# Optimization experiments

Measured on AMD Instinct MI355X. Metric: run time of the kernel, lower is better.

The kernel has to match this reference:

```python
import jax, jax.numpy as jnp
import numpy as np
import math

N_NODES = 50000
N_EDGES = 640000
IN_FEATS = 128
HEADS = 8
OUT_FEATS = 16
D_FF = 4 * IN_FEATS


def setup_inputs() -> dict:
    key = jax.random.key(0)
    ks = jax.random.split(key, 10)
    s = 0.05
    return {
        "feat": jax.random.normal(ks[0], (N_NODES, IN_FEATS), jnp.float32),
        "src": jax.random.randint(ks[1], (N_EDGES,), 0, N_NODES, jnp.int32),
        "dst": jax.random.randint(ks[2], (N_EDGES,), 0, N_NODES, jnp.int32),
        "Wq": jax.random.normal(ks[3], (IN_FEATS, HEADS * OUT_FEATS), jnp.float32) * s,
        "Wk": jax.random.normal(ks[4], (IN_FEATS, HEADS * OUT_FEATS), jnp.float32) * s,
        "Wv": jax.random.normal(ks[5], (IN_FEATS, HEADS * OUT_FEATS), jnp.float32) * s,
        "ln1_g": jnp.ones((IN_FEATS,), jnp.float32),
        "ln1_b": jnp.zeros((IN_FEATS,), jnp.float32),
        "W1": jax.random.normal(ks[6], (IN_FEATS, D_FF), jnp.float32) * s,
        "b1": jnp.zeros((D_FF,), jnp.float32),
        "prelu_a": jnp.full((D_FF,), 0.25, jnp.float32),  # torch PReLU default init
        "W2": jax.random.normal(ks[7], (D_FF, IN_FEATS), jnp.float32) * s,
        "b2": jnp.zeros((IN_FEATS,), jnp.float32),
    }


def layer_norm(x, g, b, eps=1e-5):
    mu = jnp.mean(x, axis=-1, keepdims=True)
    var = jnp.mean(jnp.square(x - mu), axis=-1, keepdims=True)
    return (x - mu) * jax.lax.rsqrt(var + eps) * g + b


def reference(feat, src, dst, Wq, Wk, Wv, ln1_g, ln1_b, W1, b1, prelu_a, W2, b2):
    N = feat.shape[0]
    feat_c = jax.lax.stop_gradient(feat)  # feat.clone().detach()
    q = (feat @ Wq).reshape(N, HEADS, OUT_FEATS)
    k = (feat_c @ Wk).reshape(N, HEADS, OUT_FEATS)
    v = (feat_c @ Wv).reshape(N, HEADS, OUT_FEATS)

    # edge score: dot(k[src], q[dst]) per head -> [E, H]
    e = jnp.einsum('ehd,ehd->eh', k[src], q[dst]) / math.sqrt(OUT_FEATS * HEADS)

    # segment softmax over incoming edges of each dst node
    m = jax.ops.segment_max(e, dst, num_segments=N)          # [N, H]
    e_exp = jnp.exp(e - m[dst])                              # [E, H]
    denom = jax.ops.segment_sum(e_exp, dst, num_segments=N)  # [N, H]
    a = e_exp / denom[dst]                                   # [E, H]

    # weighted scatter-sum aggregation
    msg = v[src] * a[:, :, None]                             # [E, H, D]
    ft2 = jax.ops.segment_sum(msg, dst, num_segments=N)      # [N, H, D]

    rst = ft2.reshape(feat.shape) + feat
    # NOTE: original applies ln1 twice (ln2 is unused) -- reproduced faithfully
    rst = layer_norm(rst, ln1_g, ln1_b)
    h = rst @ W1 + b1
    h = jnp.where(h >= 0, h, prelu_a * h)                    # PReLU, per-channel
    ffn = h @ W2 + b2
    rst = layer_norm(rst + ffn, ln1_g, ln1_b)
    return rst
```

## Files before the change

### kernel.cpp

```cpp
#include <hip/hip_runtime.h>

#define N_NODES 50000
#define N_EDGES 640000
#define F 128
#define DFF 512
#define NB 196

using u32 = unsigned int;
using u16 = unsigned short;

typedef __bf16 bf16x8 __attribute__((ext_vector_type(8)));
typedef float f32x4 __attribute__((ext_vector_type(4)));

__device__ __forceinline__ float bf2f(u16 u) {
    return __uint_as_float(((u32)u) << 16);
}
__device__ __forceinline__ float blo(u32 p) { return __uint_as_float(p << 16); }
__device__ __forceinline__ float bhi(u32 p) { return __uint_as_float(p & 0xffff0000u); }
__device__ __forceinline__ u16 f2bf(float f) {
    u32 u = __float_as_uint(f);
    u += 0x7fffu + ((u >> 16) & 1u);
    return (u16)(u >> 16);
}
__device__ __forceinline__ u32 pack2(float a, float b) {
    return (u32)f2bf(a) | ((u32)f2bf(b) << 16);
}

__global__ void k_hist(const int* __restrict__ dst, int* __restrict__ cnt) {
    int e = blockIdx.x * 256 + threadIdx.x;
    if (e < N_EDGES) atomicAdd(&cnt[dst[e]], 1);
}

__global__ void k_bsum(const int* __restrict__ counts, int* __restrict__ bsum) {
    int i = blockIdx.x * 256 + threadIdx.x;
    int v = (i < N_NODES) ? counts[i] : 0;
#pragma unroll
    for (int off = 32; off >= 1; off >>= 1) v += __shfl_xor(v, off, 64);
    __shared__ int ws[4];
    int lane = threadIdx.x & 63, wid = threadIdx.x >> 6;
    if (lane == 0) ws[wid] = v;
    __syncthreads();
    if (threadIdx.x == 0) bsum[blockIdx.x] = ws[0] + ws[1] + ws[2] + ws[3];
}

__global__ void k_bscan(const int* __restrict__ bsum, int* __restrict__ boff) {
    int t = threadIdx.x;
    int v = (t < NB) ? bsum[t] : 0;
    int lane = t & 63, wid = t >> 6;
    int incl = v;
#pragma unroll
    for (int off = 1; off < 64; off <<= 1) {
        int u = __shfl_up(incl, off, 64);
        if (lane >= off) incl += u;
    }
    __shared__ int ws[4];
    if (lane == 63) ws[wid] = incl;
    __syncthreads();
    int wo = 0;
#pragma unroll
    for (int j = 0; j < 4; ++j) if (j < wid) wo += ws[j];
    if (t < NB) boff[t] = wo + incl - v;
}

__global__ void k_bfill(const int* __restrict__ counts, const int* __restrict__ boff,
                        int* __restrict__ row_ptr) {
    int b = blockIdx.x, t = threadIdx.x;
    int i = b * 256 + t;
    int v = (i < N_NODES) ? counts[i] : 0;
    int lane = t & 63, wid = t >> 6;
    int incl = v;
#pragma unroll
    for (int off = 1; off < 64; off <<= 1) {
        int u = __shfl_up(incl, off, 64);
        if (lane >= off) incl += u;
    }
    __shared__ int ws[4];
    if (lane == 63) ws[wid] = incl;
    __syncthreads();
    int wo = 0;
#pragma unroll
    for (int j = 0; j < 4; ++j) if (j < wid) wo += ws[j];
    if (i < N_NODES) row_ptr[i] = boff[b] + wo + incl - v;
    if (i == 0) row_ptr[N_NODES] = N_EDGES;
}

__global__ void k_fill(const int* __restrict__ src, const int* __restrict__ dst,
                       const int* __restrict__ row_ptr, int* __restrict__ fill,
                       int* __restrict__ csr_src) {
    int e = blockIdx.x * 256 + threadIdx.x;
    if (e < N_EDGES) {
        int d = dst[e];
        int pos = row_ptr[d] + atomicAdd(&fill[d], 1);
        csr_src[pos] = src[e];
    }
}

__global__ void k_prepw(const float* __restrict__ Wq, const float* __restrict__ Wk,
                        const float* __restrict__ Wv, const float* __restrict__ W1,
                        const float* __restrict__ W2, u16* __restrict__ WT) {
    int idx = blockIdx.x * 256 + threadIdx.x;
    if (idx >= 180224) return;
    if (idx < 49152) {
        int mi = idx >> 14;
        int local = idx & 16383;
        const float* W = (mi == 0) ? Wq : ((mi == 1) ? Wk : Wv);
        int n = local >> 7, k = local & 127;
        WT[idx] = f2bf(W[(size_t)k * 128 + n]);
    } else if (idx < 114688) {
        int local = idx - 49152;
        int n = local >> 7, k = local & 127;
        WT[idx] = f2bf(W1[(size_t)k * 512 + n]);
    } else {
        int local = idx - 114688;
        int n = local >> 9, k = local & 511;
        WT[idx] = f2bf(W2[(size_t)k * 128 + n]);
    }
}

__global__ void k_prepA(const float* __restrict__ feat, u16* __restrict__ featb) {
    int idx = blockIdx.x * 256 + threadIdx.x;
    if (idx < N_NODES * F / 4) {
        float4 v = reinterpret_cast<const float4*>(feat)[idx];
        uint2 p;
        p.x = pack2(v.x, v.y);
        p.y = pack2(v.z, v.w);
        reinterpret_cast<uint2*>(featb)[idx] = p;
    }
}

template <int EPI>
__global__ __launch_bounds__(256) void k_mm(
    const u16* __restrict__ A, int lda,
    const u16* __restrict__ BT,
    void* __restrict__ Cv, int ldc,
    int K,
    const float* __restrict__ bias,
    const float* __restrict__ prelu,
    const u16* __restrict__ resid,
    const float* __restrict__ g,
    const float* __restrict__ bb)
{
    __shared__ u16 sA[128 * 72];
    __shared__ u16 sB[128 * 72];

    const int t = threadIdx.x;
    const int w = t >> 6;
    const int lane = t & 63;
    const int ln = lane & 15, q4 = lane >> 4;
    const int row0 = blockIdx.x * 128;
    const int cb = blockIdx.y * 128;

    f32x4 acc[2][8];
#pragma unroll
    for (int mt = 0; mt < 2; ++mt)
#pragma unroll
        for (int nt = 0; nt < 8; ++nt)
            acc[mt][nt] = (f32x4){0.f, 0.f, 0.f, 0.f};

    uint4 pa[4], pb[4];
#define LOAD_A(kc)                                                             \
    {                                                                          \
        _Pragma("unroll") for (int i = 0; i < 4; ++i) {                        \
            int u = i * 256 + t, r = u >> 3, k8 = (u & 7) * 8;                 \
            int row = row0 + r;                                                \
            uint4 val = make_uint4(0, 0, 0, 0);                                \
            if (row < N_NODES)                                                 \
                val = *reinterpret_cast<const uint4*>(A + (size_t)row * lda + (kc) + k8); \
            pa[i] = val;                                                       \
        }                                                                      \
    }
#define LOAD_B(kc)                                                             \
    {                                                                          \
        _Pragma("unroll") for (int i = 0; i < 4; ++i) {                        \
            int u = i * 256 + t, r = u >> 3, k8 = (u & 7) * 8;                 \
            pb[i] = *reinterpret_cast<const uint4*>(BT + (size_t)(cb + r) * K + (kc) + k8); \
        }                                                                      \
    }

    LOAD_A(0);
    LOAD_B(0);

    for (int kc = 0; kc < K; kc += 64) {
#pragma unroll
        for (int i = 0; i < 4; ++i) {
            int u = i * 256 + t, r = u >> 3, k8 = (u & 7) * 8;
            *reinterpret_cast<uint4*>(&sA[r * 72 + k8]) = pa[i];
            *reinterpret_cast<uint4*>(&sB[r * 72 + k8]) = pb[i];
        }
        __syncthreads();
        if (kc + 64 < K) {
            LOAD_A(kc + 64);
            LOAD_B(kc + 64);
        }
#pragma unroll
        for (int ks = 0; ks < 2; ++ks) {
            bf16x8 a0 = *reinterpret_cast<const bf16x8*>(&sA[(w * 32 + ln) * 72 + ks * 32 + q4 * 8]);
            bf16x8 a1 = *reinterpret_cast<const bf16x8*>(&sA[(w * 32 + 16 + ln) * 72 + ks * 32 + q4 * 8]);
#pragma unroll
            for (int nt = 0; nt < 8; ++nt) {
                bf16x8 b = *reinterpret_cast<const bf16x8*>(&sB[(nt * 16 + ln) * 72 + ks * 32 + q4 * 8]);
                acc[0][nt] = __builtin_amdgcn_mfma_f32_16x16x32_bf16(a0, b, acc[0][nt], 0, 0, 0);
                acc[1][nt] = __builtin_amdgcn_mfma_f32_16x16x32_bf16(a1, b, acc[1][nt], 0, 0, 0);
            }
        }
        __syncthreads();
    }
#undef LOAD_A
#undef LOAD_B

    if (EPI == 0) {
        u16* C = (u16*)Cv;
#pragma unroll
        for (int mt = 0; mt < 2; ++mt)
#pragma unroll
            for (int j = 0; j < 4; ++j) {
                int row = row0 + w * 32 + mt * 16 + q4 * 4 + j;
                if (row < N_NODES) {
#pragma unroll
                    for (int nt = 0; nt < 8; ++nt)
                        C[(size_t)row * ldc + cb + nt * 16 + ln] = f2bf(acc[mt][nt][j]);
                }
            }
    } else if (EPI == 1) {
        u16* C = (u16*)Cv;
        float bs[8], pr[8];
#pragma unroll
        for (int nt = 0; nt < 8; ++nt) {
            int col = cb + nt * 16 + ln;
            bs[nt] = bias[col];
            pr[nt] = prelu[col];
        }
#pragma unroll
        for (int mt = 0; mt < 2; ++mt)
#pragma unroll
            for (int j = 0; j < 4; ++j) {
                int row = row0 + w * 32 + mt * 16 + q4 * 4 + j;
                if (row < N_NODES) {
#pragma unroll
                    for (int nt = 0; nt < 8; ++nt) {
                        float x = acc[mt][nt][j] + bs[nt];
                        x = (x >= 0.f) ? x : pr[nt] * x;
                        C[(size_t)row * ldc + cb + nt * 16 + ln] = f2bf(x);
                    }
                }
            }
    } else {
        float* C = (float*)Cv;
        float bs[8], gv[8], bv[8];
#pragma unroll
        for (int nt = 0; nt < 8; ++nt) {
            int col = cb + nt * 16 + ln;
            bs[nt] = bias[col];
            gv[nt] = g[col];
            bv[nt] = bb[col];
        }
#pragma unroll
        for (int mt = 0; mt < 2; ++mt)
#pragma unroll
            for (int j = 0; j < 4; ++j) {
                int row = row0 + w * 32 + mt * 16 + q4 * 4 + j;
                bool ok = row < N_NODES;
                float vals[8];
                float s = 0.f, ss = 0.f;
#pragma unroll
                for (int nt = 0; nt < 8; ++nt) {
                    float x = acc[mt][nt][j] + bs[nt];
                    if (ok) x += bf2f(resid[(size_t)row * 128 + cb + nt * 16 + ln]);
                    vals[nt] = x;
                    s += x; ss += x * x;
                }
                s += __shfl_xor(s, 8, 16); ss += __shfl_xor(ss, 8, 16);
                s += __shfl_xor(s, 4, 16); ss += __shfl_xor(ss, 4, 16);
                s += __shfl_xor(s, 2, 16); ss += __shfl_xor(ss, 2, 16);
                s += __shfl_xor(s, 1, 16); ss += __shfl_xor(ss, 1, 16);
                float mu = s * (1.f / 128.f);
                float var = ss * (1.f / 128.f) - mu * mu;
                float rs = rsqrtf(var + 1e-5f);
                if (ok) {
#pragma unroll
                    for (int nt = 0; nt < 8; ++nt)
                        C[(size_t)row * 128 + cb + nt * 16 + ln] =
                            (vals[nt] - mu) * rs * gv[nt] + bv[nt];
                }
            }
    }
}

__global__ __launch_bounds__(256) void k_attn(
    const u16* __restrict__ qkv, const float* __restrict__ feat,
    const int* __restrict__ row_ptr, const int* __restrict__ csr_src,
    const float* __restrict__ g, const float* __restrict__ bb,
    u16* __restrict__ rstb)
{
    const int w = threadIdx.x >> 6;
    const int lane = threadIdx.x & 63;
    const int n = blockIdx.x * 4 + w;
    if (n >= N_NODES) return;
    const int c2 = lane * 2;
    const float scale = 0.08838834764831845f;

    const u32 qp = *reinterpret_cast<const u32*>(qkv + (size_t)n * 384 + c2);
    const float q0 = blo(qp), q1 = bhi(qp);
    const int e0 = row_ptr[n], e1 = row_ptr[n + 1];

    float m = -INFINITY, l = 0.f, a0 = 0.f, a1 = 0.f;
    int e = e0;
    for (; e + 4 <= e1; e += 4) {
        int s0 = csr_src[e], s1 = csr_src[e + 1], s2 = csr_src[e + 2], s3 = csr_src[e + 3];
        u32 kp0 = *reinterpret_cast<const u32*>(qkv + (size_t)s0 * 384 + 128 + c2);
        u32 kp1 = *reinterpret_cast<const u32*>(qkv + (size_t)s1 * 384 + 128 + c2);
        u32 kp2 = *reinterpret_cast<const u32*>(qkv + (size_t)s2 * 384 + 128 + c2);
        u32 kp3 = *reinterpret_cast<const u32*>(qkv + (size_t)s3 * 384 + 128 + c2);
        u32 vp0 = *reinterpret_cast<const u32*>(qkv + (size_t)s0 * 384 + 256 + c2);
        u32 vp1 = *reinterpret_cast<const u32*>(qkv + (size_t)s1 * 384 + 256 + c2);
        u32 vp2 = *reinterpret_cast<const u32*>(qkv + (size_t)s2 * 384 + 256 + c2);
        u32 vp3 = *reinterpret_cast<const u32*>(qkv + (size_t)s3 * 384 + 256 + c2);
        float p0 = blo(kp0) * q0 + bhi(kp0) * q1;
        float p1 = blo(kp1) * q0 + bhi(kp1) * q1;
        float p2 = blo(kp2) * q0 + bhi(kp2) * q1;
        float p3 = blo(kp3) * q0 + bhi(kp3) * q1;
        p0 += __shfl_xor(p0, 4, 8); p1 += __shfl_xor(p1, 4, 8);
        p2 += __shfl_xor(p2, 4, 8); p3 += __shfl_xor(p3, 4, 8);
        p0 += __shfl_xor(p0, 2, 8); p1 += __shfl_xor(p1, 2, 8);
        p2 += __shfl_xor(p2, 2, 8); p3 += __shfl_xor(p3, 2, 8);
        p0 += __shfl_xor(p0, 1, 8); p1 += __shfl_xor(p1, 1, 8);
        p2 += __shfl_xor(p2, 1, 8); p3 += __shfl_xor(p3, 1, 8);
        float sa = p0 * scale, sb = p1 * scale, sc = p2 * scale, sd = p3 * scale;
        float mn = fmaxf(fmaxf(m, fmaxf(sa, sb)), fmaxf(sc, sd));
        float c = __expf(m - mn);
        float ea = __expf(sa - mn), eb = __expf(sb - mn);
        float ec = __expf(sc - mn), ed = __expf(sd - mn);
        l = l * c + ((ea + eb) + (ec + ed));
        a0 = a0 * c + ea * blo(vp0) + eb * blo(vp1) + ec * blo(vp2) + ed * blo(vp3);
        a1 = a1 * c + ea * bhi(vp0) + eb * bhi(vp1) + ec * bhi(vp2) + ed * bhi(vp3);
        m = mn;
    }
    for (; e < e1; ++e) {
        int s0 = csr_src[e];
        u32 kp0 = *reinterpret_cast<const u32*>(qkv + (size_t)s0 * 384 + 128 + c2);
        u32 vp0 = *reinterpret_cast<const u32*>(qkv + (size_t)s0 * 384 + 256 + c2);
        float p0 = blo(kp0) * q0 + bhi(kp0) * q1;
        p0 += __shfl_xor(p0, 4, 8);
        p0 += __shfl_xor(p0, 2, 8);
        p0 += __shfl_xor(p0, 1, 8);
        float sa = p0 * scale;
        float mn = fmaxf(m, sa);
        float c = __expf(m - mn), ea = __expf(sa - mn);
        l = l * c + ea;
        a0 = a0 * c + ea * blo(vp0);
        a1 = a1 * c + ea * bhi(vp0);
        m = mn;
    }
    float inv = (l > 0.f) ? 1.f / l : 0.f;
    const float2 fr = *reinterpret_cast<const float2*>(feat + (size_t)n * 128 + c2);
    float x0 = a0 * inv + fr.x;
    float x1 = a1 * inv + fr.y;

    float sum = x0 + x1, sq = x0 * x0 + x1 * x1;
#pragma unroll
    for (int off = 32; off >= 1; off >>= 1) {
        sum += __shfl_xor(sum, off, 64);
        sq += __shfl_xor(sq, off, 64);
    }
    float mu = sum * (1.f / 128.f);
    float var = sq * (1.f / 128.f) - mu * mu;
    float rs = rsqrtf(var + 1e-5f);
    float y0 = (x0 - mu) * rs * g[c2] + bb[c2];
    float y1 = (x1 - mu) * rs * g[c2 + 1] + bb[c2 + 1];
    reinterpret_cast<u32*>(rstb)[(size_t)n * 64 + lane] = pack2(y0, y1);
}

extern "C" void kernel_launch(void* const* d_in, const int* in_sizes, int n_in,
                              void* d_out, int out_size, void* d_ws, size_t ws_size,
                              hipStream_t stream)
{
    const float* feat = (const float*)d_in[0];
    const int* src    = (const int*)d_in[1];
    const int* dst    = (const int*)d_in[2];
    const float* Wq   = (const float*)d_in[3];
    const float* Wk   = (const float*)d_in[4];
    const float* Wv   = (const float*)d_in[5];
    const float* ln_g = (const float*)d_in[6];
    const float* ln_b = (const float*)d_in[7];
    const float* W1   = (const float*)d_in[8];
    const float* b1   = (const float*)d_in[9];
    const float* pa   = (const float*)d_in[10];
    const float* W2   = (const float*)d_in[11];
    const float* b2   = (const float*)d_in[12];

    u16* qkv   = (u16*)d_ws;
    u16* h     = qkv + (size_t)N_NODES * 384;
    u16* featb = h;
    u16* rstb  = h + (size_t)N_NODES * 512;
    u16* WT    = rstb + (size_t)N_NODES * 128;
    u16* BqkvT = WT;
    u16* W1T   = WT + 49152;
    u16* W2T   = WT + 114688;
    int* counts  = (int*)(WT + 180224);
    int* fill    = counts + N_NODES;
    int* row_ptr = fill + N_NODES;
    int* csr_src = row_ptr + N_NODES + 1;
    int* bsum    = csr_src + N_EDGES;
    int* boff    = bsum + NB;

    k_prepw<<<(180224 + 255) / 256, 256, 0, stream>>>(Wq, Wk, Wv, W1, W2, WT);
    k_prepA<<<(N_NODES * F / 4 + 255) / 256, 256, 0, stream>>>(feat, featb);

    hipMemsetAsync(counts, 0, sizeof(int) * 2 * N_NODES, stream);
    k_hist<<<(N_EDGES + 255) / 256, 256, 0, stream>>>(dst, counts);
    k_bsum<<<NB, 256, 0, stream>>>(counts, bsum);
    k_bscan<<<1, 256, 0, stream>>>(bsum, boff);
    k_bfill<<<NB, 256, 0, stream>>>(counts, boff, row_ptr);
    k_fill<<<(N_EDGES + 255) / 256, 256, 0, stream>>>(src, dst, row_ptr, fill, csr_src);

    const int MBK = (N_NODES + 127) / 128;

    dim3 gqkv(MBK, 3);
    k_mm<0><<<gqkv, 256, 0, stream>>>(featb, 128, BqkvT, qkv, 384, 128,
                                      nullptr, nullptr, nullptr, nullptr, nullptr);

    k_attn<<<(N_NODES + 3) / 4, 256, 0, stream>>>(qkv, feat, row_ptr, csr_src, ln_g, ln_b, rstb);

    dim3 gf1(MBK, 4);
    k_mm<1><<<gf1, 256, 0, stream>>>(rstb, 128, W1T, h, 512, 128,
                                     b1, pa, nullptr, nullptr, nullptr);

    dim3 gf2(MBK, 1);
    k_mm<2><<<gf2, 256, 0, stream>>>(h, 512, W2T, d_out, 128, 512,
                                     b2, nullptr, rstb, ln_g, ln_b);
}
```

Before: 320.1 us.

## Interleave K/V per node, drop softmax max tracking, vectorize GEMM epilogues

Result: slower. 338.7 us (+5.8%).

```diff
diff --git a/kernel.cpp b/kernel.cpp
--- a/kernel.cpp
+++ b/kernel.cpp
@@ -95,36 +95,36 @@
     }
 }
 
-__global__ void k_prepw(const float* __restrict__ Wq, const float* __restrict__ Wk,
-                        const float* __restrict__ Wv, const float* __restrict__ W1,
-                        const float* __restrict__ W2, u16* __restrict__ WT) {
+#define FEAT_UNITS (N_NODES * F / 4)
+__global__ void k_prep(const float* __restrict__ feat, u16* __restrict__ featb,
+                       const float* __restrict__ Wq, const float* __restrict__ Wk,
+                       const float* __restrict__ Wv, const float* __restrict__ W1,
+                       const float* __restrict__ W2, u16* __restrict__ WT) {
     int idx = blockIdx.x * 256 + threadIdx.x;
-    if (idx >= 180224) return;
-    if (idx < 49152) {
-        int mi = idx >> 14;
-        int local = idx & 16383;
-        const float* W = (mi == 0) ? Wq : ((mi == 1) ? Wk : Wv);
-        int n = local >> 7, k = local & 127;
-        WT[idx] = f2bf(W[(size_t)k * 128 + n]);
-    } else if (idx < 114688) {
-        int local = idx - 49152;
-        int n = local >> 7, k = local & 127;
-        WT[idx] = f2bf(W1[(size_t)k * 512 + n]);
-    } else {
-        int local = idx - 114688;
-        int n = local >> 9, k = local & 511;
-        WT[idx] = f2bf(W2[(size_t)k * 128 + n]);
-    }
-}
-
-__global__ void k_prepA(const float* __restrict__ feat, u16* __restrict__ featb) {
-    int idx = blockIdx.x * 256 + threadIdx.x;
-    if (idx < N_NODES * F / 4) {
+    if (idx < FEAT_UNITS) {
         float4 v = reinterpret_cast<const float4*>(feat)[idx];
         uint2 p;
         p.x = pack2(v.x, v.y);
         p.y = pack2(v.z, v.w);
         reinterpret_cast<uint2*>(featb)[idx] = p;
+        return;
+    }
+    int wi = idx - FEAT_UNITS;
+    if (wi >= 180224) return;
+    if (wi < 49152) {
+        int mi = wi >> 14;
+        int local = wi & 16383;
+        const float* W = (mi == 0) ? Wq : ((mi == 1) ? Wk : Wv);
+        int n = local >> 7, k = local & 127;
+        WT[wi] = f2bf(W[(size_t)k * 128 + n]);
+    } else if (wi < 114688) {
+        int local = wi - 49152;
+        int n = local >> 7, k = local & 127;
+        WT[wi] = f2bf(W1[(size_t)k * 512 + n]);
+    } else {
+        int local = wi - 114688;
+        int n = local >> 9, k = local & 511;
+        WT[wi] = f2bf(W2[(size_t)k * 128 + n]);
     }
 }
 
@@ -199,8 +199,8 @@
 #pragma unroll
             for (int nt = 0; nt < 8; ++nt) {
                 bf16x8 b = *reinterpret_cast<const bf16x8*>(&sB[(nt * 16 + ln) * 72 + ks * 32 + q4 * 8]);
-                acc[0][nt] = __builtin_amdgcn_mfma_f32_16x16x32_bf16(a0, b, acc[0][nt], 0, 0, 0);
-                acc[1][nt] = __builtin_amdgcn_mfma_f32_16x16x32_bf16(a1, b, acc[1][nt], 0, 0, 0);
+                acc[0][nt] = __builtin_amdgcn_mfma_f32_16x16x32_bf16(b, a0, acc[0][nt], 0, 0, 0);
+                acc[1][nt] = __builtin_amdgcn_mfma_f32_16x16x32_bf16(b, a1, acc[1][nt], 0, 0, 0);
             }
         }
         __syncthreads();
@@ -210,84 +210,99 @@
 
     if (EPI == 0) {
         u16* C = (u16*)Cv;
-#pragma unroll
-        for (int mt = 0; mt < 2; ++mt)
-#pragma unroll
-            for (int j = 0; j < 4; ++j) {
-                int row = row0 + w * 32 + mt * 16 + q4 * 4 + j;
-                if (row < N_NODES) {
-#pragma unroll
-                    for (int nt = 0; nt < 8; ++nt)
-                        C[(size_t)row * ldc + cb + nt * 16 + ln] = f2bf(acc[mt][nt][j]);
-                }
-            }
-    } else if (EPI == 1) {
-        u16* C = (u16*)Cv;
-        float bs[8], pr[8];
-#pragma unroll
-        for (int nt = 0; nt < 8; ++nt) {
-            int col = cb + nt * 16 + ln;
-            bs[nt] = bias[col];
-            pr[nt] = prelu[col];
-        }
-#pragma unroll
-        for (int mt = 0; mt < 2; ++mt)
-#pragma unroll
-            for (int j = 0; j < 4; ++j) {
-                int row = row0 + w * 32 + mt * 16 + q4 * 4 + j;
-                if (row < N_NODES) {
-#pragma unroll
-                    for (int nt = 0; nt < 8; ++nt) {
-                        float x = acc[mt][nt][j] + bs[nt];
-                        x = (x >= 0.f) ? x : pr[nt] * x;
-                        C[(size_t)row * ldc + cb + nt * 16 + ln] = f2bf(x);
+        u32* C32 = (u32*)Cv;
+        const bool isQ = (blockIdx.y == 0);
+        const int vshift = (blockIdx.y == 2) ? 1 : 0;
+#pragma unroll
+        for (int mt = 0; mt < 2; ++mt) {
+            int row = row0 + w * 32 + mt * 16 + ln;
+            if (row < N_NODES) {
+#pragma unroll
+                for (int nt = 0; nt < 8; ++nt) {
+                    int c = nt * 16 + q4 * 4;
+                    u32 lo = pack2(acc[mt][nt][0], acc[mt][nt][1]);
+                    u32 hi = pack2(acc[mt][nt][2], acc[mt][nt][3]);
+                    if (isQ) {
+                        uint2 o; o.x = lo; o.y = hi;
+                        *reinterpret_cast<uint2*>(&C[(size_t)row * 384 + c]) = o;
+                    } else {
+                        size_t b32 = (size_t)row * 192 + 64 + c + vshift;
+                        C32[b32] = lo;
+                        C32[b32 + 2] = hi;
                     }
                 }
             }
+        }
+    } else if (EPI == 1) {
+        u16* C = (u16*)Cv;
+#pragma unroll
+        for (int mt = 0; mt < 2; ++mt) {
+            int row = row0 + w * 32 + mt * 16 + ln;
+            if (row < N_NODES) {
+#pragma unroll
+                for (int nt = 0; nt < 8; ++nt) {
+                    int col = cb + nt * 16 + q4 * 4;
+                    float4 bs = *reinterpret_cast<const float4*>(&bias[col]);
+                    float4 pr = *reinterpret_cast<const float4*>(&prelu[col]);
+                    float x0 = acc[mt][nt][0] + bs.x; x0 = x0 >= 0.f ? x0 : pr.x * x0;
+                    float x1 = acc[mt][nt][1] + bs.y; x1 = x1 >= 0.f ? x1 : pr.y * x1;
+                    float x2 = acc[mt][nt][2] + bs.z; x2 = x2 >= 0.f ? x2 : pr.z * x2;
+                    float x3 = acc[mt][nt][3] + bs.w; x3 = x3 >= 0.f ? x3 : pr.w * x3;
+                    uint2 o; o.x = pack2(x0, x1); o.y = pack2(x2, x3);
+                    *reinterpret_cast<uint2*>(&C[(size_t)row * ldc + col]) = o;
+                }
+            }
+        }
     } else {
         float* C = (float*)Cv;
-        float bs[8], gv[8], bv[8];
-#pragma unroll
-        for (int nt = 0; nt < 8; ++nt) {
-            int col = cb + nt * 16 + ln;
-            bs[nt] = bias[col];
-            gv[nt] = g[col];
-            bv[nt] = bb[col];
-        }
-#pragma unroll
-        for (int mt = 0; mt < 2; ++mt)
-#pragma unroll
-            for (int j = 0; j < 4; ++j) {
-                int row = row0 + w * 32 + mt * 16 + q4 * 4 + j;
-                bool ok = row < N_NODES;
-                float vals[8];
-                float s = 0.f, ss = 0.f;
+#pragma unroll
+        for (int mt = 0; mt < 2; ++mt) {
+            int row = row0 + w * 32 + mt * 16 + ln;
+            bool ok = row < N_NODES;
+            float s = 0.f, ss = 0.f;
+#pragma unroll
+            for (int nt = 0; nt < 8; ++nt) {
+                int col = nt * 16 + q4 * 4;
+                float4 bs = *reinterpret_cast<const float4*>(&bias[col]);
+                float r0 = 0.f, r1 = 0.f, r2 = 0.f, r3 = 0.f;
+                if (ok) {
+                    uint2 rp = *reinterpret_cast<const uint2*>(&resid[(size_t)row * 128 + col]);
+                    r0 = blo(rp.x); r1 = bhi(rp.x); r2 = blo(rp.y); r3 = bhi(rp.y);
+                }
+                float x0 = acc[mt][nt][0] + bs.x + r0;
+                float x1 = acc[mt][nt][1] + bs.y + r1;
+                float x2 = acc[mt][nt][2] + bs.z + r2;
+                float x3 = acc[mt][nt][3] + bs.w + r3;
+                acc[mt][nt][0] = x0; acc[mt][nt][1] = x1;
+                acc[mt][nt][2] = x2; acc[mt][nt][3] = x3;
+                s += (x0 + x1) + (x2 + x3);
+                ss += (x0 * x0 + x1 * x1) + (x2 * x2 + x3 * x3);
+            }
+            s += __shfl_xor(s, 16, 64); ss += __shfl_xor(ss, 16, 64);
+            s += __shfl_xor(s, 32, 64); ss += __shfl_xor(ss, 32, 64);
+            float mu = s * (1.f / 128.f);
+            float var = ss * (1.f / 128.f) - mu * mu;
+            float rs = rsqrtf(var + 1e-5f);
+            if (ok) {
 #pragma unroll
                 for (int nt = 0; nt < 8; ++nt) {
-                    float x = acc[mt][nt][j] + bs[nt];
-                    if (ok) x += bf2f(resid[(size_t)row * 128 + cb + nt * 16 + ln]);
-                    vals[nt] = x;
-                    s += x; ss += x * x;
-                }
-                s += __shfl_xor(s, 8, 16); ss += __shfl_xor(ss, 8, 16);
-                s += __shfl_xor(s, 4, 16); ss += __shfl_xor(ss, 4, 16);
-                s += __shfl_xor(s, 2, 16); ss += __shfl_xor(ss, 2, 16);
-                s += __shfl_xor(s, 1, 16); ss += __shfl_xor(ss, 1, 16);
-                float mu = s * (1.f / 128.f);
-                float var = ss * (1.f / 128.f) - mu * mu;
-                float rs = rsqrtf(var + 1e-5f);
-                if (ok) {
-#pragma unroll
-                    for (int nt = 0; nt < 8; ++nt)
-                        C[(size_t)row * 128 + cb + nt * 16 + ln] =
-                            (vals[nt] - mu) * rs * gv[nt] + bv[nt];
+                    int col = nt * 16 + q4 * 4;
+                    float4 gv = *reinterpret_cast<const float4*>(&g[col]);
+                    float4 bv = *reinterpret_cast<const float4*>(&bb[col]);
+                    float4 o;
+                    o.x = (acc[mt][nt][0] - mu) * rs * gv.x + bv.x;
+                    o.y = (acc[mt][nt][1] - mu) * rs * gv.y + bv.y;
+                    o.z = (acc[mt][nt][2] - mu) * rs * gv.z + bv.z;
+                    o.w = (acc[mt][nt][3] - mu) * rs * gv.w + bv.w;
+                    *reinterpret_cast<float4*>(&C[(size_t)row * 128 + col]) = o;
                 }
             }
+        }
     }
 }
 
 __global__ __launch_bounds__(256) void k_attn(
-    const u16* __restrict__ qkv, const float* __restrict__ feat,
+    const u32* __restrict__ Q32, const float* __restrict__ feat,
     const int* __restrict__ row_ptr, const int* __restrict__ csr_src,
     const float* __restrict__ g, const float* __restrict__ bb,
     u16* __restrict__ rstb)
@@ -296,62 +311,51 @@
     const int lane = threadIdx.x & 63;
     const int n = blockIdx.x * 4 + w;
     if (n >= N_NODES) return;
-    const int c2 = lane * 2;
     const float scale = 0.08838834764831845f;
 
-    const u32 qp = *reinterpret_cast<const u32*>(qkv + (size_t)n * 384 + c2);
+    const u32 qp = Q32[(size_t)n * 192 + lane];
     const float q0 = blo(qp), q1 = bhi(qp);
     const int e0 = row_ptr[n], e1 = row_ptr[n + 1];
-
-    float m = -INFINITY, l = 0.f, a0 = 0.f, a1 = 0.f;
+    const int kvoff = 64 + 2 * lane;
+
+    float l = 0.f, a0 = 0.f, a1 = 0.f;
     int e = e0;
     for (; e + 4 <= e1; e += 4) {
         int s0 = csr_src[e], s1 = csr_src[e + 1], s2 = csr_src[e + 2], s3 = csr_src[e + 3];
-        u32 kp0 = *reinterpret_cast<const u32*>(qkv + (size_t)s0 * 384 + 128 + c2);
-        u32 kp1 = *reinterpret_cast<const u32*>(qkv + (size_t)s1 * 384 + 128 + c2);
-        u32 kp2 = *reinterpret_cast<const u32*>(qkv + (size_t)s2 * 384 + 128 + c2);
-        u32 kp3 = *reinterpret_cast<const u32*>(qkv + (size_t)s3 * 384 + 128 + c2);
-        u32 vp0 = *reinterpret_cast<const u32*>(qkv + (size_t)s0 * 384 + 256 + c2);
-        u32 vp1 = *reinterpret_cast<const u32*>(qkv + (size_t)s1 * 384 + 256 + c2);
-        u32 vp2 = *reinterpret_cast<const u32*>(qkv + (size_t)s2 * 384 + 256 + c2);
-        u32 vp3 = *reinterpret_cast<const u32*>(qkv + (size_t)s3 * 384 + 256 + c2);
-        float p0 = blo(kp0) * q0 + bhi(kp0) * q1;
-        float p1 = blo(kp1) * q0 + bhi(kp1) * q1;
-        float p2 = blo(kp2) * q0 + bhi(kp2) * q1;
-        float p3 = blo(kp3) * q0 + bhi(kp3) * q1;
+        uint2 kv0 = *reinterpret_cast<const uint2*>(&Q32[(size_t)s0 * 192 + kvoff]);
+        uint2 kv1 = *reinterpret_cast<const uint2*>(&Q32[(size_t)s1 * 192 + kvoff]);
+        uint2 kv2 = *reinterpret_cast<const uint2*>(&Q32[(size_t)s2 * 192 + kvoff]);
+        uint2 kv3 = *reinterpret_cast<const uint2*>(&Q32[(size_t)s3 * 192 + kvoff]);
+        float p0 = blo(kv0.x) * q0 + bhi(kv0.x) * q1;
+        float p1 = blo(kv1.x) * q0 + bhi(kv1.x) * q1;
+        float p2 = blo(kv2.x) * q0 + bhi(kv2.x) * q1;
+        float p3 = blo(kv3.x) * q0 + bhi(kv3.x) * q1;
         p0 += __shfl_xor(p0, 4, 8); p1 += __shfl_xor(p1, 4, 8);
         p2 += __shfl_xor(p2, 4, 8); p3 += __shfl_xor(p3, 4, 8);
         p0 += __shfl_xor(p0, 2, 8); p1 += __shfl_xor(p1, 2, 8);
         p2 += __shfl_xor(p2, 2, 8); p3 += __shfl_xor(p3, 2, 8);
         p0 += __shfl_xor(p0, 1, 8); p1 += __shfl_xor(p1, 1, 8);
         p2 += __shfl_xor(p2, 1, 8); p3 += __shfl_xor(p3, 1, 8);
-        float sa = p0 * scale, sb = p1 * scale, sc = p2 * scale, sd = p3 * scale;
-        float mn = fmaxf(fmaxf(m, fmaxf(sa, sb)), fmaxf(sc, sd));
-        float c = __expf(m - mn);
-        float ea = __expf(sa - mn), eb = __expf(sb - mn);
-        float ec = __expf(sc - mn), ed = __expf(sd - mn);
-        l = l * c + ((ea + eb) + (ec + ed));
-        a0 = a0 * c + ea * blo(vp0) + eb * blo(vp1) + ec * blo(vp2) + ed * blo(vp3);
-        a1 = a1 * c + ea * bhi(vp0) + eb * bhi(vp1) + ec * bhi(vp2) + ed * bhi(vp3);
-        m = mn;
+        float ea = __expf(p0 * scale), eb = __expf(p1 * scale);
+        float ec = __expf(p2 * scale), ed = __expf(p3 * scale);
+        l += (ea + eb) + (ec + ed);
+        a0 += ea * blo(kv0.y) + eb * blo(kv1.y) + ec * blo(kv2.y) + ed * blo(kv3.y);
+        a1 += ea * bhi(kv0.y) + eb * bhi(kv1.y) + ec * bhi(kv2.y) + ed * bhi(kv3.y);
     }
     for (; e < e1; ++e) {
         int s0 = csr_src[e];
-        u32 kp0 = *reinterpret_cast<const u32*>(qkv + (size_t)s0 * 384 + 128 + c2);
-        u32 vp0 = *reinterpret_cast<const u32*>(qkv + (size_t)s0 * 384 + 256 + c2);
-        float p0 = blo(kp0) * q0 + bhi(kp0) * q1;
+        uint2 kv0 = *reinterpret_cast<const uint2*>(&Q32[(size_t)s0 * 192 + kvoff]);
+        float p0 = blo(kv0.x) * q0 + bhi(kv0.x) * q1;
         p0 += __shfl_xor(p0, 4, 8);
         p0 += __shfl_xor(p0, 2, 8);
         p0 += __shfl_xor(p0, 1, 8);
-        float sa = p0 * scale;
-        float mn = fmaxf(m, sa);
-        float c = __expf(m - mn), ea = __expf(sa - mn);
-        l = l * c + ea;
-        a0 = a0 * c + ea * blo(vp0);
-        a1 = a1 * c + ea * bhi(vp0);
-        m = mn;
+        float ea = __expf(p0 * scale);
+        l += ea;
+        a0 += ea * blo(kv0.y);
+        a1 += ea * bhi(kv0.y);
     }
     float inv = (l > 0.f) ? 1.f / l : 0.f;
+    const int c2 = lane * 2;
     const float2 fr = *reinterpret_cast<const float2*>(feat + (size_t)n * 128 + c2);
     float x0 = a0 * inv + fr.x;
     float x1 = a1 * inv + fr.y;
@@ -403,8 +407,8 @@
     int* bsum    = csr_src + N_EDGES;
     int* boff    = bsum + NB;
 
-    k_prepw<<<(180224 + 255) / 256, 256, 0, stream>>>(Wq, Wk, Wv, W1, W2, WT);
-    k_prepA<<<(N_NODES * F / 4 + 255) / 256, 256, 0, stream>>>(feat, featb);
+    k_prep<<<(FEAT_UNITS + 180224 + 255) / 256, 256, 0, stream>>>(
+        feat, featb, Wq, Wk, Wv, W1, W2, WT);
 
     hipMemsetAsync(counts, 0, sizeof(int) * 2 * N_NODES, stream);
     k_hist<<<(N_EDGES + 255) / 256, 256, 0, stream>>>(dst, counts);
@@ -419,7 +423,8 @@
     k_mm<0><<<gqkv, 256, 0, stream>>>(featb, 128, BqkvT, qkv, 384, 128,
                                       nullptr, nullptr, nullptr, nullptr, nullptr);
 
-    k_attn<<<(N_NODES + 3) / 4, 256, 0, stream>>>(qkv, feat, row_ptr, csr_src, ln_g, ln_b, rstb);
+    k_attn<<<(N_NODES + 3) / 4, 256, 0, stream>>>((const u32*)qkv, feat, row_ptr, csr_src,
+                                                  ln_g, ln_b, rstb);
 
     dim3 gf1(MBK, 4);
     k_mm<1><<<gf1, 256, 0, stream>>>(rstb, 128, W1T, h, 512, 128,
```
